# Kernel tuning notes

Hardware: AMD Instinct MI355X
Metric: run time of the kernel (lower is better)

The kernel has to match this reference:

```python
import jax, jax.numpy as jnp
import numpy as np

N, E = 50000, 400000
IN_DIM = OUT_DIM = 256
H, DK = 8, 32
NT, ET = 6, 3
LN_EPS = 1e-5


def setup_inputs() -> dict:
    key = jax.random.key(0)
    ks = jax.random.split(key, 16)
    glorot = lambda k, shape: jax.random.normal(k, shape, jnp.float32) * np.sqrt(2.0 / (shape[-2] + shape[-1]))
    return {
        "node_features": jax.random.normal(ks[0], (N, IN_DIM), jnp.float32),
        "edge_index": jax.random.randint(ks[1], (2, E), 0, N, jnp.int32),
        "edge_features": jax.random.normal(ks[2], (E, 16), jnp.float32),
        "node_types": jax.random.randint(ks[3], (N,), 0, NT, jnp.int32),
        "edge_types": jax.random.randint(ks[4], (E,), 0, ET, jnp.int32),
        # type-specific projection weights stored [T, in, out] (y = x @ W + b)
        "Wk": glorot(ks[5], (NT, IN_DIM, OUT_DIM)), "bk": jnp.zeros((NT, OUT_DIM), jnp.float32),
        "Wq": glorot(ks[6], (NT, IN_DIM, OUT_DIM)), "bq": jnp.zeros((NT, OUT_DIM), jnp.float32),
        "Wv": glorot(ks[7], (NT, IN_DIM, OUT_DIM)), "bv": jnp.zeros((NT, OUT_DIM), jnp.float32),
        "relation_pri": jnp.ones((ET, H), jnp.float32),
        # relation transforms, no bias, stored [T, dk_in, dk_out]
        "Wa": glorot(ks[8], (ET, DK, DK)),
        "Wm": glorot(ks[9], (ET, DK, DK)),
        "ln_g": jnp.ones((OUT_DIM,), jnp.float32),
        "ln_b": jnp.zeros((OUT_DIM,), jnp.float32),
    }


def _type_proj(x, node_types, W, b):
    # compute all 6 type projections, then select per node (faithful to masked loop)
    y_all = jnp.einsum("ni,tio->tno", x, W) + b[:, None, :]  # [T, N, out]
    return y_all[node_types, jnp.arange(x.shape[0])]         # [N, out]


def _forward(node_features, edge_index, node_types, edge_types,
             Wk, bk, Wq, bq, Wv, bv, relation_pri, Wa, Wm, ln_g, ln_b):
    n = node_features.shape[0]
    K = _type_proj(node_features, node_types, Wk, bk).reshape(n, H, DK)
    Q = _type_proj(node_features, node_types, Wq, bq).reshape(n, H, DK)
    V = _type_proj(node_features, node_types, Wv, bv).reshape(n, H, DK)

    src, tgt = edge_index[0], edge_index[1]
    Ks, Qt, Vs = K[src], Q[tgt], V[src]  # [E, H, dk]
    inv_sqrt_dk = 1.0 / np.sqrt(DK).astype(np.float32)

    msgs = jnp.zeros((edge_types.shape[0], H, DK), jnp.float32)
    for t in range(ET):  # small fixed loop over edge types
        mask = edge_types == t                              # [E]
        Ke = jnp.einsum("ehd,dk->ehk", Ks, Wa[t])           # relation_att
        Ve = jnp.einsum("ehd,dk->ehk", Vs, Wm[t])           # relation_msg
        scores = jnp.sum(Ke * Qt, -1) * inv_sqrt_dk * relation_pri[t]  # [E, H]
        scores = jnp.where(mask[:, None], scores, -jnp.inf)
        w = jax.nn.softmax(scores, axis=0)                  # softmax over ALL edges of this type
        msgs = msgs + jnp.where(mask[:, None, None], w[..., None] * Ve, 0.0)

    agg = jax.ops.segment_sum(msgs.reshape(-1, OUT_DIM), tgt, num_segments=n)  # index_add_
    out = agg + node_features                               # skip = Identity (in_dim == out_dim)
    mu = jnp.mean(out, -1, keepdims=True)
    var = jnp.var(out, -1, keepdims=True)
    return (out - mu) * jax.lax.rsqrt(var + LN_EPS) * ln_g + ln_b


def reference(node_features, edge_index, edge_features, node_types, edge_types,
              Wk, bk, Wq, bq, Wv, bv, relation_pri, Wa, Wm, ln_g, ln_b):
    # edge_features are unused by the original forward; dropout is eval-mode identity
    return _forward(node_features, edge_index, node_types, edge_types,
                    Wk, bk, Wq, bq, Wv, bv, relation_pri, Wa, Wm, ln_g, ln_b)
```

## Files before the change

### kernel.cpp

```cpp
#include <hip/hip_runtime.h>
#include <math.h>

#define H_    8
#define DK_   32
#define NT_   6
#define ET_   3
#define DIM_  256
#define LN_EPS 1e-5f
#define NMATS (NT_ * 7)
#define NBLK  2048
#define NBIN  (ET_ * H_)
#define NSTEP 56
#define TROWS 128
#define MAXNB 1024

typedef __attribute__((ext_vector_type(8))) short short8v;
typedef __attribute__((ext_vector_type(4))) float f32x4;
typedef __attribute__((ext_vector_type(2))) float f32x2;

__device__ __forceinline__ unsigned short f2bf(float f){
    unsigned u = __float_as_uint(f);
    return (unsigned short)((u + 0x7fffu + ((u >> 16) & 1u)) >> 16);
}
__device__ __forceinline__ float bflo(unsigned u){ return __uint_as_float(u << 16); }
__device__ __forceinline__ float bfhi(unsigned u){ return __uint_as_float(u & 0xFFFF0000u); }
__device__ __forceinline__ float bf2f(unsigned short v){ return __uint_as_float((unsigned)v << 16); }

__device__ __forceinline__ unsigned char f2fp8(float f){
    int r = __builtin_amdgcn_cvt_pk_fp8_f32(f, f, 0, false);
    return (unsigned char)(r & 0xFF);
}

__global__ __launch_bounds__(256) void k_hist(const int* __restrict__ ntyp, int n,
                                              int* __restrict__ bhist){
    const int tid = threadIdx.x;
    const int gi = blockIdx.x * 256 + tid;
    const int wave = tid >> 6, lane = tid & 63;
    const int t = (gi < n) ? ntyp[gi] : -1;
    __shared__ int whist[4][8];
    #pragma unroll
    for (int tt = 0; tt < NT_; tt++){
        unsigned long long bal = __ballot(t == tt);
        if (lane == 0) whist[wave][tt] = __popcll(bal);
    }
    __syncthreads();
    if (tid < NT_)
        bhist[blockIdx.x * 8 + tid] =
            whist[0][tid] + whist[1][tid] + whist[2][tid] + whist[3][tid];
}

__global__ __launch_bounds__(256) void k_scanhist(int* __restrict__ bhist, int nb,
                                                  int* __restrict__ offs, int* __restrict__ meta){
    __shared__ int hh[MAXNB * 8 / 4];
    __shared__ int tot[8], toff[8], tbase[8], ntl_s;
    const int tid = threadIdx.x;

    for (int i = tid; i < nb * 8; i += 256) hh[i] = bhist[i];
    __syncthreads();

    if (tid < 8){
        int run = 0;
        for (int b = 0; b < nb; b++){
            int c = hh[b * 8 + tid];
            hh[b * 8 + tid] = run;
            run += c;
        }
        tot[tid] = run;
    }
    __syncthreads();

    if (tid == 0){
        int off = 0, tb = 0;
        for (int tt = 0; tt < NT_; tt++){
            toff[tt] = off;
            tbase[tt] = tb;
            tb += (tot[tt] + TROWS - 1) / TROWS;
            off += tot[tt];
        }
        for (int tt = NT_; tt < 8; tt++){ toff[tt] = 0; tbase[tt] = tb; }
        ntl_s = tb;
        meta[0] = tb;
    }
    __syncthreads();

    for (int i = tid; i < ntl_s; i += 256){
        int t = 0;
        #pragma unroll
        for (int tt = 1; tt < NT_; tt++) if (i >= tbase[tt]) t = tt;
        const int k = i - tbase[t];
        const int rem = tot[t] - k * TROWS;
        meta[1 + 3*i]     = t;
        meta[1 + 3*i + 1] = toff[t] + k * TROWS;
        meta[1 + 3*i + 2] = (rem < TROWS) ? rem : TROWS;
    }
    if (tid < NT_) offs[tid] = toff[tid];

    for (int i = tid; i < nb * 8; i += 256)
        bhist[i] = hh[i] + toff[i & 7];
}

__global__ __launch_bounds__(256) void k_scatter2(const int* __restrict__ ntyp, int n,
                                                  const int* __restrict__ bhist,
                                                  int* __restrict__ sorted){
    const int tid = threadIdx.x;
    const int gi = blockIdx.x * 256 + tid;
    const int wave = tid >> 6, lane = tid & 63;
    const int t = (gi < n) ? ntyp[gi] : -1;
    __shared__ int whist[4][8];
    unsigned long long mybal = 0;
    #pragma unroll
    for (int tt = 0; tt < NT_; tt++){
        unsigned long long bal = __ballot(t == tt);
        if (lane == 0) whist[wave][tt] = __popcll(bal);
        if (t == tt) mybal = bal;
    }
    __syncthreads();
    if (gi < n){
        int wo = 0;
        for (int w = 0; w < wave; w++) wo += whist[w][t];
        const unsigned long long below = (lane == 0) ? 0ULL : (~0ULL >> (64 - lane));
        const int rank = bhist[blockIdx.x * 8 + t] + wo + __popcll(mybal & below);
        sorted[rank] = gi;
    }
}

__global__ __launch_bounds__(256) void k_pack(
    const float* __restrict__ Wq, const float* __restrict__ Wk, const float* __restrict__ Wv,
    const float* __restrict__ Wa, const float* __restrict__ Wm, const float* __restrict__ pri,
    unsigned short* __restrict__ pw)
{
    const int gid = blockIdx.x * 256 + threadIdx.x;
    if (gid >= NMATS * 8 * 16 * 64) return;
    const int l = gid & 63;
    const int j = (gid >> 6) & 15;
    const int p = (gid >> 10) & 7;
    const int matg = gid >> 13;
    const int tn = matg / 7, m = matg % 7;
    const int col = j * 16 + (l & 15);
    const int k0  = p * 32 + (l >> 4) * 8;
    const int h = col >> 5, c = col & 31;

    float vals[8];
    if (m == 0){
        #pragma unroll
        for (int i = 0; i < 8; i++)
            vals[i] = Wq[((size_t)tn * 256 + (k0 + i)) * 256 + col];
    } else if (m <= 3){
        const int te = m - 1;
        const float scale = 0.17677669529663687f * pri[te * H_ + h];
        #pragma unroll
        for (int i = 0; i < 8; i++){
            const float* wk = Wk + ((size_t)tn * 256 + (k0 + i)) * 256 + h * 32;
            const float* wa = Wa + (size_t)te * 1024 + c;
            float s = 0.f;
            for (int d = 0; d < 32; d++) s = fmaf(wk[d], wa[d * 32], s);
            vals[i] = s * scale;
        }
    } else {
        const int te = m - 4;
        #pragma unroll
        for (int i = 0; i < 8; i++){
            const float* wv = Wv + ((size_t)tn * 256 + (k0 + i)) * 256 + h * 32;
            const float* wm = Wm + (size_t)te * 1024 + c;
            float s = 0.f;
            for (int d = 0; d < 32; d++) s = fmaf(wv[d], wm[d * 32], s);
            vals[i] = s;
        }
    }
    unsigned short o[8];
    #pragma unroll
    for (int i = 0; i < 8; i++) o[i] = f2bf(vals[i]);
    *reinterpret_cast<uint4*>(pw + (size_t)gid * 8) = *reinterpret_cast<const uint4*>(o);
}

__global__ void k_bias(
    const float* __restrict__ bq, const float* __restrict__ bk, const float* __restrict__ bv,
    const float* __restrict__ Wa, const float* __restrict__ Wm, const float* __restrict__ pri,
    float* __restrict__ bpack)
{
    const int gid = blockIdx.x * 256 + threadIdx.x;
    if (gid >= NMATS * 256) return;
    const int col = gid & 255;
    const int matg = gid >> 8;
    const int tn = matg / 7, m = matg % 7;
    const int h = col >> 5, c = col & 31;
    float v;
    if (m == 0) v = bq[tn * 256 + col];
    else if (m <= 3){
        const int te = m - 1;
        float s = 0.f;
        for (int d = 0; d < 32; d++) s = fmaf(bk[tn * 256 + h * 32 + d], Wa[te * 1024 + d * 32 + c], s);
        v = s * 0.17677669529663687f * pri[te * H_ + h];
    } else {
        const int te = m - 4;
        float s = 0.f;
        for (int d = 0; d < 32; d++) s = fmaf(bv[tn * 256 + h * 32 + d], Wm[te * 1024 + d * 32 + c], s);
        v = s;
    }
    bpack[gid] = v;
}

__global__ __launch_bounds__(512, 2) void k_proj(
    const float* __restrict__ x, const int* __restrict__ sorted, const int* __restrict__ meta,
    const unsigned short* __restrict__ pw, const float* __restrict__ bpack,
    unsigned short* __restrict__ Qb, unsigned char* __restrict__ Ktb, unsigned char* __restrict__ Vtb)
{
    const int ntl = meta[0];
    if ((int)blockIdx.x >= ntl) return;
    const int q = ntl >> 3, r = ntl & 7;
    const int xcd = blockIdx.x & 7, ii = blockIdx.x >> 3;
    const int tile = (xcd < r) ? xcd * (q + 1) + ii
                               : r * (q + 1) + (xcd - r) * q + ii;
    const int tn    = meta[1 + 3*tile];
    const int start = meta[1 + 3*tile + 1];
    const int rows  = meta[1 + 3*tile + 2];

    __shared__ unsigned short xs[TROWS * 256];
    __shared__ int ids[TROWS];
    const int tid = threadIdx.x;
    if (tid < TROWS) ids[tid] = sorted[start + ((tid < rows) ? tid : 0)];
    __syncthreads();

    char* xb = reinterpret_cast<char*>(xs);
    for (int idx = tid; idx < TROWS * 32; idx += 512){
        const int r2 = idx >> 5, c16 = idx & 31;
        const float* src = x + (size_t)ids[r2] * DIM_ + c16 * 8;
        float4 a = *reinterpret_cast<const float4*>(src);
        float4 b = *reinterpret_cast<const float4*>(src + 4);
        unsigned short o[8] = {f2bf(a.x), f2bf(a.y), f2bf(a.z), f2bf(a.w),
                               f2bf(b.x), f2bf(b.y), f2bf(b.z), f2bf(b.w)};
        const int byte = r2 * 512 + ((c16 * 16) ^ ((r2 & 7) << 4));
        *reinterpret_cast<uint4*>(xb + byte) = *reinterpret_cast<const uint4*>(o);
    }
    __syncthreads();

    const int wid = tid >> 6, l = tid & 63;
    const int rg = wid >> 2;
    const int cg = wid & 3;
    const int l15 = l & 15, lg = l >> 4;
    const int xorv = (l15 & 7) << 4;
    const size_t matbase = (size_t)tn * 7;
    const int rowbase = rg * 64;

    f32x4 acc[4][4];
    short8v b0[4], b1[4];

    {
        const unsigned short* sp0 = pw + matbase * 8 * 8192;
        #pragma unroll
        for (int j = 0; j < 4; j++)
            b0[j] = *reinterpret_cast<const short8v*>(sp0 + (cg * 4 + j) * 512 + l * 8);
    }

    auto proj_step = [&](const int s, short8v (&cur)[4], short8v (&pf)[4]){
        const int m = s >> 3, p = s & 7;
        const int matg = (int)matbase + m;

        if (s + 1 < NSTEP){
            const unsigned short* sp = pw + (matbase * 8 + (s + 1)) * 8192;
            #pragma unroll
            for (int j = 0; j < 4; j++)
                pf[j] = *reinterpret_cast<const short8v*>(sp + (cg * 4 + j) * 512 + l * 8);
        }

        if (p == 0){
            #pragma unroll
            for (int j = 0; j < 4; j++){
                const float bj = bpack[matg * 256 + cg * 64 + j * 16 + l15];
                #pragma unroll
                for (int i = 0; i < 4; i++) acc[i][j] = (f32x4){bj, bj, bj, bj};
            }
        }

        {
            short8v a[4];
            const int kb = (p * 64 + (lg << 4)) ^ xorv;
            #pragma unroll
            for (int i = 0; i < 4; i++)
                a[i] = *reinterpret_cast<const short8v*>(xb + (rowbase + i * 16 + l15) * 512 + kb);
            #pragma unroll
            for (int i = 0; i < 4; i++)
                #pragma unroll
                for (int j = 0; j < 4; j++)
                    acc[i][j] = __builtin_amdgcn_mfma_f32_16x16x32_bf16(a[i], cur[j], acc[i][j], 0, 0, 0);
        }

        if (p == 7){
            #pragma unroll
            for (int i = 0; i < 4; i++){
                #pragma unroll
                for (int rr = 0; rr < 4; rr++){
                    const int row = rowbase + i * 16 + lg * 4 + rr;
                    if (row < rows){
                        const size_t node = (size_t)ids[row];
                        if (m == 0){
                            unsigned short* optr = Qb + node * 256 + cg * 64 + l15;
                            #pragma unroll
                            for (int j = 0; j < 4; j++) optr[j * 16] = f2bf(acc[i][j][rr]);
                        } else {
                            unsigned char* optr = ((m <= 3) ? Ktb + node * 768 + (size_t)(m - 1) * 256
                                                            : Vtb + node * 768 + (size_t)(m - 4) * 256)
                                                  + cg * 64 + l15;
                            #pragma unroll
                            for (int j = 0; j < 4; j++) optr[j * 16] = f2fp8(acc[i][j][rr]);
                        }
                    }
                }
            }
        }
    };

    for (int s = 0; s < NSTEP; s += 2){
        proj_step(s,     b0, b1);
        proj_step(s + 1, b1, b0);
    }
}

__global__ void k_ecount(const int* __restrict__ ei, int E_, int* __restrict__ ecnt){
    int e = blockIdx.x * blockDim.x + threadIdx.x;
    if (e < E_) atomicAdd(&ecnt[ei[E_ + e]], 1);
}

__global__ __launch_bounds__(256) void k_scan1(const int* __restrict__ ecnt, int n,
                                               int* __restrict__ excl, int* __restrict__ bsum){
    __shared__ int sh[256];
    const int tid = threadIdx.x;
    const int gi = blockIdx.x * 256 + tid;
    int v = (gi < n) ? ecnt[gi] : 0;
    sh[tid] = v;
    __syncthreads();
    for (int off = 1; off < 256; off <<= 1){
        int t = (tid >= off) ? sh[tid - off] : 0;
        __syncthreads();
        sh[tid] += t;
        __syncthreads();
    }
    if (gi < n) excl[gi] = sh[tid] - v;
    if (tid == 255) bsum[blockIdx.x] = sh[255];
}

__global__ __launch_bounds__(256) void k_scan2(int* __restrict__ bsum, int nb){
    __shared__ int sh[MAXNB];
    const int tid = threadIdx.x;
    for (int i = tid; i < nb; i += 256) sh[i] = bsum[i];
    __syncthreads();
    if (tid == 0){
        int run = 0;
        for (int b = 0; b < nb; b++){ int c = sh[b]; sh[b] = run; run += c; }
    }
    __syncthreads();
    for (int i = tid; i < nb; i += 256) bsum[i] = sh[i];
}

__global__ __launch_bounds__(256) void k_scan3(int n, int E_, const int* __restrict__ bsum,
                                               int* __restrict__ eoff, int* __restrict__ cursor){
    const int gi = blockIdx.x * 256 + threadIdx.x;
    if (gi < n){
        int v = eoff[gi] + bsum[blockIdx.x];
        eoff[gi] = v;
        cursor[gi] = v;
    }
    if (gi == 0) eoff[n] = E_;
}

__global__ void k_escatter(const int* __restrict__ ei, const int* __restrict__ etyp, int E_,
                           int* __restrict__ cursor, int2* __restrict__ ep){
    int e = blockIdx.x * blockDim.x + threadIdx.x;
    if (e < E_){
        int tg = ei[E_ + e];
        int pos = atomicAdd(&cursor[tg], 1);
        ep[pos] = make_int2(ei[e] | (etyp[e] << 28), tg);
    }
}

__global__ __launch_bounds__(256) void k_score(
    const unsigned char* __restrict__ Ktb, const unsigned short* __restrict__ Qb,
    const int2* __restrict__ ep,
    unsigned short* __restrict__ SC, float* __restrict__ psum, int EH)
{
    const int tid = threadIdx.x;
    float s0 = 0.f, s1 = 0.f, s2 = 0.f;

    for (int idx = blockIdx.x * 256 + tid; idx < EH; idx += NBLK * 256){
        const int pos = idx >> 3, h = idx & 7;
        const int2 pr = ep[pos];
        const int s = pr.x & 0x0FFFFFFF, t = pr.x >> 28;
        const int tg = pr.y;
        const unsigned char*  kp = Ktb + ((size_t)s * 3 + t) * 256 + h * 32;
        const unsigned short* qp = Qb + (size_t)tg * 256 + h * 32;
        uint4 k8a = *reinterpret_cast<const uint4*>(kp);
        uint4 k8b = *reinterpret_cast<const uint4*>(kp + 16);
        unsigned kw[8] = {k8a.x, k8a.y, k8a.z, k8a.w, k8b.x, k8b.y, k8b.z, k8b.w};
        uint4 qa = *reinterpret_cast<const uint4*>(qp);
        uint4 qb = *reinterpret_cast<const uint4*>(qp + 8);
        uint4 qc = *reinterpret_cast<const uint4*>(qp + 16);
        uint4 qd = *reinterpret_cast<const uint4*>(qp + 24);
        unsigned qw[16] = {qa.x, qa.y, qa.z, qa.w, qb.x, qb.y, qb.z, qb.w,
                           qc.x, qc.y, qc.z, qc.w, qd.x, qd.y, qd.z, qd.w};
        float acc = 0.f;
        #pragma unroll
        for (int w = 0; w < 8; w++){
            f32x2 lo = __builtin_amdgcn_cvt_pk_f32_fp8(kw[w], false);
            f32x2 hi = __builtin_amdgcn_cvt_pk_f32_fp8(kw[w], true);
            acc = fmaf(lo.x, bflo(qw[2*w]),   acc);
            acc = fmaf(lo.y, bfhi(qw[2*w]),   acc);
            acc = fmaf(hi.x, bflo(qw[2*w+1]), acc);
            acc = fmaf(hi.y, bfhi(qw[2*w+1]), acc);
        }
        const float e = __expf(acc);
        SC[idx] = f2bf(e);
        s0 += (t == 0) ? e : 0.f;
        s1 += (t == 1) ? e : 0.f;
        s2 += (t == 2) ? e : 0.f;
    }

    #pragma unroll
    for (int s = 8; s <= 32; s <<= 1){
        s0 += __shfl_xor(s0, s, 64);
        s1 += __shfl_xor(s1, s, 64);
        s2 += __shfl_xor(s2, s, 64);
    }
    __shared__ float sm[4][NBIN];
    const int wave = tid >> 6, lane = tid & 63;
    if (lane < 8){ sm[wave][lane] = s0; sm[wave][8 + lane] = s1; sm[wave][16 + lane] = s2; }
    __syncthreads();
    if (tid < NBIN)
        psum[blockIdx.x * NBIN + tid] = sm[0][tid] + sm[1][tid] + sm[2][tid] + sm[3][tid];
}

__global__ __launch_bounds__(256) void k_redsum(const float* __restrict__ psum,
                                                float* __restrict__ rw){
    const int b = blockIdx.x, tid = threadIdx.x;
    float s = 0.f;
    for (int i = tid; i < NBLK; i += 256) s += psum[i * NBIN + b];
    #pragma unroll
    for (int m = 1; m < 64; m <<= 1) s += __shfl_xor(s, m, 64);
    __shared__ float sm[4];
    if ((tid & 63) == 0) sm[tid >> 6] = s;
    __syncthreads();
    if (tid == 0){
        float t = sm[0] + sm[1] + sm[2] + sm[3];
        rw[b] = (t > 0.f) ? 1.f / t : 0.f;
    }
}

__global__ __launch_bounds__(256) void k_aggln(
    const unsigned char* __restrict__ Vtb, const float* __restrict__ x,
    const int* __restrict__ eoff, const int2* __restrict__ ep,
    const unsigned short* __restrict__ SC, const float* __restrict__ rw,
    const float* __restrict__ g, const float* __restrict__ b,
    float* __restrict__ out, int n)
{
    const int idx = blockIdx.x * 256 + threadIdx.x;
    if (idx >= n * H_) return;
    const int tg = idx >> 3, h = idx & 7;

    const float rw0 = rw[h], rw1 = rw[8 + h], rw2 = rw[16 + h];

    float acc[DK_];
    #pragma unroll
    for (int k = 0; k < DK_; k++) acc[k] = 0.f;

    const int p1 = eoff[tg + 1];
    for (int pos = eoff[tg]; pos < p1; ++pos){
        const int pl = ep[pos].x;
        const int s = pl & 0x0FFFFFFF, t = pl >> 28;
        const float rwv = (t == 0) ? rw0 : (t == 1) ? rw1 : rw2;
        const float w = bf2f(SC[pos * 8 + h]) * rwv;
        const unsigned char* vp = Vtb + ((size_t)s * 3 + t) * 256 + h * 32;
        uint4 v8a = *reinterpret_cast<const uint4*>(vp);
        uint4 v8b = *reinterpret_cast<const uint4*>(vp + 16);
        unsigned vw[8] = {v8a.x, v8a.y, v8a.z, v8a.w, v8b.x, v8b.y, v8b.z, v8b.w};
        #pragma unroll
        for (int q = 0; q < 8; q++){
            f32x2 lo = __builtin_amdgcn_cvt_pk_f32_fp8(vw[q], false);
            f32x2 hi = __builtin_amdgcn_cvt_pk_f32_fp8(vw[q], true);
            acc[4*q+0] = fmaf(w, lo.x, acc[4*q+0]);
            acc[4*q+1] = fmaf(w, lo.y, acc[4*q+1]);
            acc[4*q+2] = fmaf(w, hi.x, acc[4*q+2]);
            acc[4*q+3] = fmaf(w, hi.y, acc[4*q+3]);
        }
    }

    #pragma unroll
    for (int k4 = 0; k4 < 8; k4++){
        float4 x4 = *reinterpret_cast<const float4*>(x + (size_t)tg * DIM_ + h * DK_ + k4 * 4);
        acc[4*k4] += x4.x; acc[4*k4+1] += x4.y; acc[4*k4+2] += x4.z; acc[4*k4+3] += x4.w;
    }

    float s1 = 0.f, s2 = 0.f;
    #pragma unroll
    for (int k = 0; k < DK_; k++){ s1 += acc[k]; s2 = fmaf(acc[k], acc[k], s2); }
    #pragma unroll
    for (int m = 1; m <= 4; m <<= 1){
        s1 += __shfl_xor(s1, m, 64);
        s2 += __shfl_xor(s2, m, 64);
    }
    const float mu  = s1 * (1.f / DIM_);
    const float var = s2 * (1.f / DIM_) - mu * mu;
    const float rs  = rsqrtf(var + LN_EPS);

    float* __restrict__ o = out + (size_t)tg * DIM_ + h * DK_;
    #pragma unroll
    for (int k4 = 0; k4 < 8; k4++){
        float4 g4 = *reinterpret_cast<const float4*>(g + h * DK_ + k4 * 4);
        float4 b4 = *reinterpret_cast<const float4*>(b + h * DK_ + k4 * 4);
        float4 o4;
        o4.x = (acc[4*k4]   - mu) * rs * g4.x + b4.x;
        o4.y = (acc[4*k4+1] - mu) * rs * g4.y + b4.y;
        o4.z = (acc[4*k4+2] - mu) * rs * g4.z + b4.z;
        o4.w = (acc[4*k4+3] - mu) * rs * g4.w + b4.w;
        *reinterpret_cast<float4*>(o + k4 * 4) = o4;
    }
}

extern "C" void kernel_launch(void* const* d_in, const int* in_sizes, int n_in,
                              void* d_out, int out_size, void* d_ws, size_t ws_size,
                              hipStream_t stream)
{
    const float* x   = (const float*)d_in[0];
    const int*  ei   = (const int*)d_in[1];
    const int*  ntyp = (const int*)d_in[3];
    const int*  etyp = (const int*)d_in[4];
    const float* Wk  = (const float*)d_in[5];
    const float* bk  = (const float*)d_in[6];
    const float* Wq  = (const float*)d_in[7];
    const float* bq  = (const float*)d_in[8];
    const float* Wv  = (const float*)d_in[9];
    const float* bv  = (const float*)d_in[10];
    const float* pri = (const float*)d_in[11];
    const float* Wa  = (const float*)d_in[12];
    const float* Wm  = (const float*)d_in[13];
    const float* lg  = (const float*)d_in[14];
    const float* lb  = (const float*)d_in[15];

    const int n  = in_sizes[0] / DIM_;
    const int E_ = in_sizes[4];
    const int EH = E_ * H_;
    float* out = (float*)d_out;

    const size_t NF = (size_t)n * DIM_;
    unsigned short* Qb  = (unsigned short*)d_ws;
    unsigned char*  Ktb = (unsigned char*)(Qb + NF);
    unsigned char*  Vtb = Ktb + NF * 3;
    unsigned short* pwp = (unsigned short*)(Vtb + NF * 3);
    unsigned short* SC  = pwp + (size_t)NMATS * 65536;
    float* bpack = (float*)(SC + (size_t)EH);
    float* psum  = bpack + NMATS * 256;
    float* rw    = psum + (size_t)NBLK * NBIN;
    int* sorted  = (int*)(rw + NBIN);
    int* offsN   = sorted + n;
    const int NB = (n + 255) / 256;
    int* bhist   = offsN + 8;
    int* meta    = bhist + (size_t)NB * 8;
    const int maxtiles = (n + TROWS - 1) / TROWS + NT_;
    int* ecnt    = meta + 1 + 3 * maxtiles;
    int* eoff    = ecnt + n;
    int* cursorE = eoff + n + 1;
    int* bsum    = cursorE + n;
    int2* ep     = (int2*)(bsum + 1024);

    hipMemsetAsync(ecnt, 0, (size_t)n * sizeof(int), stream);

    k_pack<<<(NMATS * 8 * 16 * 64 + 255) / 256, 256, 0, stream>>>(Wq, Wk, Wv, Wa, Wm, pri, pwp);
    k_bias<<<(NMATS * 256 + 255) / 256, 256, 0, stream>>>(bq, bk, bv, Wa, Wm, pri, bpack);

    k_hist    <<<NB, 256, 0, stream>>>(ntyp, n, bhist);
    k_scanhist<<<1, 256, 0, stream>>>(bhist, NB, offsN, meta);
    k_scatter2<<<NB, 256, 0, stream>>>(ntyp, n, bhist, sorted);
    k_proj    <<<maxtiles, 512, 0, stream>>>(x, sorted, meta, pwp, bpack, Qb, Ktb, Vtb);

    k_ecount  <<<(E_ + 255) / 256, 256, 0, stream>>>(ei, E_, ecnt);
    k_scan1   <<<NB, 256, 0, stream>>>(ecnt, n, eoff, bsum);
    k_scan2   <<<1, 256, 0, stream>>>(bsum, NB);
    k_scan3   <<<NB, 256, 0, stream>>>(n, E_, bsum, eoff, cursorE);
    k_escatter<<<(E_ + 255) / 256, 256, 0, stream>>>(ei, etyp, E_, cursorE, ep);

    k_score <<<NBLK, 256, 0, stream>>>(Ktb, Qb, ep, SC, psum, EH);
    k_redsum<<<NBIN, 256, 0, stream>>>(psum, rw);
    k_aggln <<<(n * H_ + 255) / 256, 256, 0, stream>>>(Vtb, x, eoff, ep, SC, rw, lg, lb, out, n);
}
```

Measured before the change: 246.6 us.

## Fuse preprocessing kernels and merge edge scatter into score computation

Merges pack and bias into one launch, merges the node-type histogram with the edge in-degree count, fuses the node scatter with the first edge-offset scan, and folds the edge scatter into the score kernel, which now computes all 8 heads per edge thread. Edge records shrink from int2 to int, and per-block softmax partial sums go through shared-memory float atomics. The aim is to cut kernel launches and intermediate global round trips. In exchange, the score kernel loses per-head parallelism, meaning fewer threads with more serial work and less coalesced Q/K loads, and it adds shared-memory atomic contention.

```diff
diff --git a/kernel.cpp b/kernel.cpp
--- a/kernel.cpp
+++ b/kernel.cpp
@@ -8,11 +8,13 @@
 #define DIM_  256
 #define LN_EPS 1e-5f
 #define NMATS (NT_ * 7)
-#define NBLK  2048
 #define NBIN  (ET_ * H_)
 #define NSTEP 56
 #define TROWS 128
 #define MAXNB 1024
+#define ESB   1024
+#define PACKN (NMATS * 8 * 16 * 64)
+#define BIASN (NMATS * 256)
 
 typedef __attribute__((ext_vector_type(8))) short short8v;
 typedef __attribute__((ext_vector_type(4))) float f32x4;
@@ -31,22 +33,28 @@
     return (unsigned char)(r & 0xFF);
 }
 
-__global__ __launch_bounds__(256) void k_hist(const int* __restrict__ ntyp, int n,
-                                              int* __restrict__ bhist){
+__global__ __launch_bounds__(256) void k_histcount(
+    const int* __restrict__ ntyp, int n, int* __restrict__ bhist, int nb,
+    const int* __restrict__ ei, int E_, int* __restrict__ ecnt)
+{
     const int tid = threadIdx.x;
-    const int gi = blockIdx.x * 256 + tid;
-    const int wave = tid >> 6, lane = tid & 63;
-    const int t = (gi < n) ? ntyp[gi] : -1;
-    __shared__ int whist[4][8];
-    #pragma unroll
-    for (int tt = 0; tt < NT_; tt++){
-        unsigned long long bal = __ballot(t == tt);
-        if (lane == 0) whist[wave][tt] = __popcll(bal);
-    }
-    __syncthreads();
-    if (tid < NT_)
-        bhist[blockIdx.x * 8 + tid] =
-            whist[0][tid] + whist[1][tid] + whist[2][tid] + whist[3][tid];
+    if ((int)blockIdx.x < nb){
+        const int gi = blockIdx.x * 256 + tid;
+        const int wave = tid >> 6, lane = tid & 63;
+        const int t = (gi < n) ? ntyp[gi] : -1;
+        __shared__ int whist[4][8];
+        #pragma unroll
+        for (int tt = 0; tt < NT_; tt++){
+            unsigned long long bal = __ballot(t == tt);
+            if (lane == 0) whist[wave][tt] = __popcll(bal);
+        }
+        __syncthreads();
+        if (tid < NT_)
+            bhist[blockIdx.x * 8 + tid] =
+                whist[0][tid] + whist[1][tid] + whist[2][tid] + whist[3][tid];
+    }
+    for (int e = blockIdx.x * 256 + tid; e < E_; e += ESB * 256)
+        atomicAdd(&ecnt[ei[E_ + e]], 1);
 }
 
 __global__ __launch_bounds__(256) void k_scanhist(int* __restrict__ bhist, int nb,
@@ -99,9 +107,11 @@
         bhist[i] = hh[i] + toff[i & 7];
 }
 
-__global__ __launch_bounds__(256) void k_scatter2(const int* __restrict__ ntyp, int n,
-                                                  const int* __restrict__ bhist,
-                                                  int* __restrict__ sorted){
+__global__ __launch_bounds__(256) void k_scatscan(
+    const int* __restrict__ ntyp, int n, const int* __restrict__ bhist,
+    int* __restrict__ sorted,
+    const int* __restrict__ ecnt, int* __restrict__ eoff, int* __restrict__ bsum)
+{
     const int tid = threadIdx.x;
     const int gi = blockIdx.x * 256 + tid;
     const int wave = tid >> 6, lane = tid & 63;
@@ -122,82 +132,91 @@
         const int rank = bhist[blockIdx.x * 8 + t] + wo + __popcll(mybal & below);
         sorted[rank] = gi;
     }
-}
-
-__global__ __launch_bounds__(256) void k_pack(
+    __shared__ int sh[256];
+    int v = (gi < n) ? ecnt[gi] : 0;
+    __syncthreads();
+    sh[tid] = v;
+    __syncthreads();
+    for (int off = 1; off < 256; off <<= 1){
+        int tv = (tid >= off) ? sh[tid - off] : 0;
+        __syncthreads();
+        sh[tid] += tv;
+        __syncthreads();
+    }
+    if (gi < n) eoff[gi] = sh[tid] - v;
+    if (tid == 255) bsum[blockIdx.x] = sh[255];
+}
+
+__global__ __launch_bounds__(256) void k_packbias(
     const float* __restrict__ Wq, const float* __restrict__ Wk, const float* __restrict__ Wv,
     const float* __restrict__ Wa, const float* __restrict__ Wm, const float* __restrict__ pri,
-    unsigned short* __restrict__ pw)
-{
-    const int gid = blockIdx.x * 256 + threadIdx.x;
-    if (gid >= NMATS * 8 * 16 * 64) return;
-    const int l = gid & 63;
-    const int j = (gid >> 6) & 15;
-    const int p = (gid >> 10) & 7;
-    const int matg = gid >> 13;
-    const int tn = matg / 7, m = matg % 7;
-    const int col = j * 16 + (l & 15);
-    const int k0  = p * 32 + (l >> 4) * 8;
-    const int h = col >> 5, c = col & 31;
-
-    float vals[8];
-    if (m == 0){
+    const float* __restrict__ bq, const float* __restrict__ bk, const float* __restrict__ bv,
+    unsigned short* __restrict__ pw, float* __restrict__ bpack)
+{
+    const int gid0 = blockIdx.x * 256 + threadIdx.x;
+    if (gid0 < PACKN){
+        const int gid = gid0;
+        const int l = gid & 63;
+        const int j = (gid >> 6) & 15;
+        const int p = (gid >> 10) & 7;
+        const int matg = gid >> 13;
+        const int tn = matg / 7, m = matg % 7;
+        const int col = j * 16 + (l & 15);
+        const int k0  = p * 32 + (l >> 4) * 8;
+        const int h = col >> 5, c = col & 31;
+
+        float vals[8];
+        if (m == 0){
+            #pragma unroll
+            for (int i = 0; i < 8; i++)
+                vals[i] = Wq[((size_t)tn * 256 + (k0 + i)) * 256 + col];
+        } else if (m <= 3){
+            const int te = m - 1;
+            const float scale = 0.17677669529663687f * pri[te * H_ + h];
+            #pragma unroll
+            for (int i = 0; i < 8; i++){
+                const float* wk = Wk + ((size_t)tn * 256 + (k0 + i)) * 256 + h * 32;
+                const float* wa = Wa + (size_t)te * 1024 + c;
+                float s = 0.f;
+                for (int d = 0; d < 32; d++) s = fmaf(wk[d], wa[d * 32], s);
+                vals[i] = s * scale;
+            }
+        } else {
+            const int te = m - 4;
+            #pragma unroll
+            for (int i = 0; i < 8; i++){
+                const float* wv = Wv + ((size_t)tn * 256 + (k0 + i)) * 256 + h * 32;
+                const float* wm = Wm + (size_t)te * 1024 + c;
+                float s = 0.f;
+                for (int d = 0; d < 32; d++) s = fmaf(wv[d], wm[d * 32], s);
+                vals[i] = s;
+            }
+        }
+        unsigned short o[8];
         #pragma unroll
-        for (int i = 0; i < 8; i++)
-            vals[i] = Wq[((size_t)tn * 256 + (k0 + i)) * 256 + col];
-    } else if (m <= 3){
-        const int te = m - 1;
-        const float scale = 0.17677669529663687f * pri[te * H_ + h];
-        #pragma unroll
-        for (int i = 0; i < 8; i++){
-            const float* wk = Wk + ((size_t)tn * 256 + (k0 + i)) * 256 + h * 32;
-            const float* wa = Wa + (size_t)te * 1024 + c;
+        for (int i = 0; i < 8; i++) o[i] = f2bf(vals[i]);
+        *reinterpret_cast<uint4*>(pw + (size_t)gid * 8) = *reinterpret_cast<const uint4*>(o);
+    } else if (gid0 < PACKN + BIASN){
+        const int gid = gid0 - PACKN;
+        const int col = gid & 255;
+        const int matg = gid >> 8;
+        const int tn = matg / 7, m = matg % 7;
+        const int h = col >> 5, c = col & 31;
+        float v;
+        if (m == 0) v = bq[tn * 256 + col];
+        else if (m <= 3){
+            const int te = m - 1;
             float s = 0.f;
-            for (int d = 0; d < 32; d++) s = fmaf(wk[d], wa[d * 32], s);
-            vals[i] = s * scale;
-        }
-    } else {
-        const int te = m - 4;
-        #pragma unroll
-        for (int i = 0; i < 8; i++){
-            const float* wv = Wv + ((size_t)tn * 256 + (k0 + i)) * 256 + h * 32;
-            const float* wm = Wm + (size_t)te * 1024 + c;
+            for (int d = 0; d < 32; d++) s = fmaf(bk[tn * 256 + h * 32 + d], Wa[te * 1024 + d * 32 + c], s);
+            v = s * 0.17677669529663687f * pri[te * H_ + h];
+        } else {
+            const int te = m - 4;
             float s = 0.f;
-            for (int d = 0; d < 32; d++) s = fmaf(wv[d], wm[d * 32], s);
-            vals[i] = s;
-        }
-    }
-    unsigned short o[8];
-    #pragma unroll
-    for (int i = 0; i < 8; i++) o[i] = f2bf(vals[i]);
-    *reinterpret_cast<uint4*>(pw + (size_t)gid * 8) = *reinterpret_cast<const uint4*>(o);
-}
-
-__global__ void k_bias(
-    const float* __restrict__ bq, const float* __restrict__ bk, const float* __restrict__ bv,
-    const float* __restrict__ Wa, const float* __restrict__ Wm, const float* __restrict__ pri,
-    float* __restrict__ bpack)
-{
-    const int gid = blockIdx.x * 256 + threadIdx.x;
-    if (gid >= NMATS * 256) return;
-    const int col = gid & 255;
-    const int matg = gid >> 8;
-    const int tn = matg / 7, m = matg % 7;
-    const int h = col >> 5, c = col & 31;
-    float v;
-    if (m == 0) v = bq[tn * 256 + col];
-    else if (m <= 3){
-        const int te = m - 1;
-        float s = 0.f;
-        for (int d = 0; d < 32; d++) s = fmaf(bk[tn * 256 + h * 32 + d], Wa[te * 1024 + d * 32 + c], s);
-        v = s * 0.17677669529663687f * pri[te * H_ + h];
-    } else {
-        const int te = m - 4;
-        float s = 0.f;
-        for (int d = 0; d < 32; d++) s = fmaf(bv[tn * 256 + h * 32 + d], Wm[te * 1024 + d * 32 + c], s);
-        v = s;
-    }
-    bpack[gid] = v;
+            for (int d = 0; d < 32; d++) s = fmaf(bv[tn * 256 + h * 32 + d], Wm[te * 1024 + d * 32 + c], s);
+            v = s;
+        }
+        bpack[gid] = v;
+    }
 }
 
 __global__ __launch_bounds__(512, 2) void k_proj(
@@ -316,29 +335,6 @@
     }
 }
 
-__global__ void k_ecount(const int* __restrict__ ei, int E_, int* __restrict__ ecnt){
-    int e = blockIdx.x * blockDim.x + threadIdx.x;
-    if (e < E_) atomicAdd(&ecnt[ei[E_ + e]], 1);
-}
-
-__global__ __launch_bounds__(256) void k_scan1(const int* __restrict__ ecnt, int n,
-                                               int* __restrict__ excl, int* __restrict__ bsum){
-    __shared__ int sh[256];
-    const int tid = threadIdx.x;
-    const int gi = blockIdx.x * 256 + tid;
-    int v = (gi < n) ? ecnt[gi] : 0;
-    sh[tid] = v;
-    __syncthreads();
-    for (int off = 1; off < 256; off <<= 1){
-        int t = (tid >= off) ? sh[tid - off] : 0;
-        __syncthreads();
-        sh[tid] += t;
-        __syncthreads();
-    }
-    if (gi < n) excl[gi] = sh[tid] - v;
-    if (tid == 255) bsum[blockIdx.x] = sh[255];
-}
-
 __global__ __launch_bounds__(256) void k_scan2(int* __restrict__ bsum, int nb){
     __shared__ int sh[MAXNB];
     const int tid = threadIdx.x;
@@ -363,76 +359,61 @@
     if (gi == 0) eoff[n] = E_;
 }
 
-__global__ void k_escatter(const int* __restrict__ ei, const int* __restrict__ etyp, int E_,
-                           int* __restrict__ cursor, int2* __restrict__ ep){
-    int e = blockIdx.x * blockDim.x + threadIdx.x;
-    if (e < E_){
-        int tg = ei[E_ + e];
-        int pos = atomicAdd(&cursor[tg], 1);
-        ep[pos] = make_int2(ei[e] | (etyp[e] << 28), tg);
-    }
-}
-
-__global__ __launch_bounds__(256) void k_score(
+__global__ __launch_bounds__(256) void k_esc_score(
+    const int* __restrict__ ei, const int* __restrict__ etyp, int E_,
+    int* __restrict__ cursor,
     const unsigned char* __restrict__ Ktb, const unsigned short* __restrict__ Qb,
-    const int2* __restrict__ ep,
-    unsigned short* __restrict__ SC, float* __restrict__ psum, int EH)
-{
+    int* __restrict__ ep, unsigned short* __restrict__ SC, float* __restrict__ psum)
+{
+    __shared__ float bins[NBIN];
     const int tid = threadIdx.x;
-    float s0 = 0.f, s1 = 0.f, s2 = 0.f;
-
-    for (int idx = blockIdx.x * 256 + tid; idx < EH; idx += NBLK * 256){
-        const int pos = idx >> 3, h = idx & 7;
-        const int2 pr = ep[pos];
-        const int s = pr.x & 0x0FFFFFFF, t = pr.x >> 28;
-        const int tg = pr.y;
-        const unsigned char*  kp = Ktb + ((size_t)s * 3 + t) * 256 + h * 32;
-        const unsigned short* qp = Qb + (size_t)tg * 256 + h * 32;
-        uint4 k8a = *reinterpret_cast<const uint4*>(kp);
-        uint4 k8b = *reinterpret_cast<const uint4*>(kp + 16);
-        unsigned kw[8] = {k8a.x, k8a.y, k8a.z, k8a.w, k8b.x, k8b.y, k8b.z, k8b.w};
-        uint4 qa = *reinterpret_cast<const uint4*>(qp);
-        uint4 qb = *reinterpret_cast<const uint4*>(qp + 8);
-        uint4 qc = *reinterpret_cast<const uint4*>(qp + 16);
-        uint4 qd = *reinterpret_cast<const uint4*>(qp + 24);
-        unsigned qw[16] = {qa.x, qa.y, qa.z, qa.w, qb.x, qb.y, qb.z, qb.w,
-                           qc.x, qc.y, qc.z, qc.w, qd.x, qd.y, qd.z, qd.w};
-        float acc = 0.f;
-        #pragma unroll
-        for (int w = 0; w < 8; w++){
-            f32x2 lo = __builtin_amdgcn_cvt_pk_f32_fp8(kw[w], false);
-            f32x2 hi = __builtin_amdgcn_cvt_pk_f32_fp8(kw[w], true);
-            acc = fmaf(lo.x, bflo(qw[2*w]),   acc);
-            acc = fmaf(lo.y, bfhi(qw[2*w]),   acc);
-            acc = fmaf(hi.x, bflo(qw[2*w+1]), acc);
-            acc = fmaf(hi.y, bfhi(qw[2*w+1]), acc);
-        }
-        const float e = __expf(acc);
-        SC[idx] = f2bf(e);
-        s0 += (t == 0) ? e : 0.f;
-        s1 += (t == 1) ? e : 0.f;
-        s2 += (t == 2) ? e : 0.f;
-    }
-
-    #pragma unroll
-    for (int s = 8; s <= 32; s <<= 1){
-        s0 += __shfl_xor(s0, s, 64);
-        s1 += __shfl_xor(s1, s, 64);
-        s2 += __shfl_xor(s2, s, 64);
-    }
-    __shared__ float sm[4][NBIN];
-    const int wave = tid >> 6, lane = tid & 63;
-    if (lane < 8){ sm[wave][lane] = s0; sm[wave][8 + lane] = s1; sm[wave][16 + lane] = s2; }
-    __syncthreads();
-    if (tid < NBIN)
-        psum[blockIdx.x * NBIN + tid] = sm[0][tid] + sm[1][tid] + sm[2][tid] + sm[3][tid];
+    if (tid < NBIN) bins[tid] = 0.f;
+    __syncthreads();
+
+    for (int e = blockIdx.x * 256 + tid; e < E_; e += ESB * 256){
+        const int tg = ei[E_ + e];
+        const int t  = etyp[e];
+        const int s  = ei[e];
+        const int pos = atomicAdd(&cursor[tg], 1);
+        ep[pos] = s | (t << 28);
+        const unsigned char*  kp = Ktb + ((size_t)s * 3 + t) * 256;
+        const unsigned short* qp = Qb + (size_t)tg * 256;
+        for (int h = 0; h < H_; h++){
+            const unsigned char*  kh = kp + h * 32;
+            const unsigned short* qh = qp + h * 32;
+            uint4 k8a = *reinterpret_cast<const uint4*>(kh);
+            uint4 k8b = *reinterpret_cast<const uint4*>(kh + 16);
+            unsigned kw[8] = {k8a.x, k8a.y, k8a.z, k8a.w, k8b.x, k8b.y, k8b.z, k8b.w};
+            uint4 qa = *reinterpret_cast<const uint4*>(qh);
+            uint4 qb = *reinterpret_cast<const uint4*>(qh + 8);
+            uint4 qc = *reinterpret_cast<const uint4*>(qh + 16);
+            uint4 qd = *reinterpret_cast<const uint4*>(qh + 24);
+            unsigned qw[16] = {qa.x, qa.y, qa.z, qa.w, qb.x, qb.y, qb.z, qb.w,
+                               qc.x, qc.y, qc.z, qc.w, qd.x, qd.y, qd.z, qd.w};
+            float acc = 0.f;
+            #pragma unroll
+            for (int w = 0; w < 8; w++){
+                f32x2 lo = __builtin_amdgcn_cvt_pk_f32_fp8(kw[w], false);
+                f32x2 hi = __builtin_amdgcn_cvt_pk_f32_fp8(kw[w], true);
+                acc = fmaf(lo.x, bflo(qw[2*w]),   acc);
+                acc = fmaf(lo.y, bfhi(qw[2*w]),   acc);
+                acc = fmaf(hi.x, bflo(qw[2*w+1]), acc);
+                acc = fmaf(hi.y, bfhi(qw[2*w+1]), acc);
+            }
+            const float ev = __expf(acc);
+            SC[(size_t)pos * 8 + h] = f2bf(ev);
+            atomicAdd(&bins[t * 8 + h], ev);
+        }
+    }
+    __syncthreads();
+    if (tid < NBIN) psum[blockIdx.x * NBIN + tid] = bins[tid];
 }
 
 __global__ __launch_bounds__(256) void k_redsum(const float* __restrict__ psum,
                                                 float* __restrict__ rw){
     const int b = blockIdx.x, tid = threadIdx.x;
     float s = 0.f;
-    for (int i = tid; i < NBLK; i += 256) s += psum[i * NBIN + b];
+    for (int i = tid; i < ESB; i += 256) s += psum[i * NBIN + b];
     #pragma unroll
     for (int m = 1; m < 64; m <<= 1) s += __shfl_xor(s, m, 64);
     __shared__ float sm[4];
@@ -446,7 +427,7 @@
 
 __global__ __launch_bounds__(256) void k_aggln(
     const unsigned char* __restrict__ Vtb, const float* __restrict__ x,
-    const int* __restrict__ eoff, const int2* __restrict__ ep,
+    const int* __restrict__ eoff, const int* __restrict__ ep,
     const unsigned short* __restrict__ SC, const float* __restrict__ rw,
     const float* __restrict__ g, const float* __restrict__ b,
     float* __restrict__ out, int n)
@@ -463,10 +444,10 @@
 
     const int p1 = eoff[tg + 1];
     for (int pos = eoff[tg]; pos < p1; ++pos){
-        const int pl = ep[pos].x;
+        const int pl = ep[pos];
         const int s = pl & 0x0FFFFFFF, t = pl >> 28;
         const float rwv = (t == 0) ? rw0 : (t == 1) ? rw1 : rw2;
-        const float w = bf2f(SC[pos * 8 + h]) * rwv;
+        const float w = bf2f(SC[(size_t)pos * 8 + h]) * rwv;
         const unsigned char* vp = Vtb + ((size_t)s * 3 + t) * 256 + h * 32;
         uint4 v8a = *reinterpret_cast<const uint4*>(vp);
         uint4 v8b = *reinterpret_cast<const uint4*>(vp + 16);
@@ -547,7 +528,7 @@
     unsigned short* SC  = pwp + (size_t)NMATS * 65536;
     float* bpack = (float*)(SC + (size_t)EH);
     float* psum  = bpack + NMATS * 256;
-    float* rw    = psum + (size_t)NBLK * NBIN;
+    float* rw    = psum + (size_t)ESB * NBIN;
     int* sorted  = (int*)(rw + NBIN);
     int* offsN   = sorted + n;
     const int NB = (n + 255) / 256;
@@ -558,25 +539,22 @@
     int* eoff    = ecnt + n;
     int* cursorE = eoff + n + 1;
     int* bsum    = cursorE + n;
-    int2* ep     = (int2*)(bsum + 1024);
+    int* ep      = bsum + 1024;
 
     hipMemsetAsync(ecnt, 0, (size_t)n * sizeof(int), stream);
 
-    k_pack<<<(NMATS * 8 * 16 * 64 + 255) / 256, 256, 0, stream>>>(Wq, Wk, Wv, Wa, Wm, pri, pwp);
-    k_bias<<<(NMATS * 256 + 255) / 256, 256, 0, stream>>>(bq, bk, bv, Wa, Wm, pri, bpack);
-
-    k_hist    <<<NB, 256, 0, stream>>>(ntyp, n, bhist);
-    k_scanhist<<<1, 256, 0, stream>>>(bhist, NB, offsN, meta);
-    k_scatter2<<<NB, 256, 0, stream>>>(ntyp, n, bhist, sorted);
-    k_proj    <<<maxtiles, 512, 0, stream>>>(x, sorted, meta, pwp, bpack, Qb, Ktb, Vtb);
-
-    k_ecount  <<<(E_ + 255) / 256, 256, 0, stream>>>(ei, E_, ecnt);
-    k_scan1   <<<NB, 256, 0, stream>>>(ecnt, n, eoff, bsum);
-    k_scan2   <<<1, 256, 0, stream>>>(bsum, NB);
-    k_scan3   <<<NB, 256, 0, stream>>>(n, E_, bsum, eoff, cursorE);
-    k_escatter<<<(E_ + 255) / 256, 256, 0, stream>>>(ei, etyp, E_, cursorE, ep);
-
-    k_score <<<NBLK, 256, 0, stream>>>(Ktb, Qb, ep, SC, psum, EH);
-    k_redsum<<<NBIN, 256, 0, stream>>>(psum, rw);
-    k_aggln <<<(n * H_ + 255) / 256, 256, 0, stream>>>(Vtb, x, eoff, ep, SC, rw, lg, lb, out, n);
-}
+    k_packbias<<<(PACKN + BIASN + 255) / 256, 256, 0, stream>>>(
+        Wq, Wk, Wv, Wa, Wm, pri, bq, bk, bv, pwp, bpack);
+
+    k_histcount<<<ESB, 256, 0, stream>>>(ntyp, n, bhist, NB, ei, E_, ecnt);
+    k_scanhist <<<1, 256, 0, stream>>>(bhist, NB, offsN, meta);
+    k_scatscan <<<NB, 256, 0, stream>>>(ntyp, n, bhist, sorted, ecnt, eoff, bsum);
+    k_scan2    <<<1, 256, 0, stream>>>(bsum, NB);
+    k_scan3    <<<NB, 256, 0, stream>>>(n, E_, bsum, eoff, cursorE);
+
+    k_proj<<<maxtiles, 512, 0, stream>>>(x, sorted, meta, pwp, bpack, Qb, Ktb, Vtb);
+
+    k_esc_score<<<ESB, 256, 0, stream>>>(ei, etyp, E_, cursorE, Ktb, Qb, ep, SC, psum);
+    k_redsum   <<<NBIN, 256, 0, stream>>>(psum, rw);
+    k_aggln    <<<(n * H_ + 255) / 256, 256, 0, stream>>>(Vtb, x, eoff, ep, SC, rw, lg, lb, out, n);
+}
```

Measured after the change: 279.0 us. 1.13x slower.
